# Kernel tuning notes

Hardware: AMD Instinct MI355X
Metric: run time of the kernel (lower is better)

## Reference

```python
import jax, jax.numpy as jnp
import numpy as np

FEATURE_DIM = 512
NUM_HEADS = 8
HEAD_DIM = FEATURE_DIM // NUM_HEADS
B, L = 4, 2048


def setup_inputs() -> dict:
    key = jax.random.key(0)
    ks = jax.random.split(key, 10)
    s = 1.0 / np.sqrt(FEATURE_DIM)
    inp = {
        "ppg": jax.random.normal(ks[0], (B, FEATURE_DIM, L), dtype=jnp.float32),
        "ecg": jax.random.normal(ks[1], (B, FEATURE_DIM, L), dtype=jnp.float32),
        "Wq": jax.random.uniform(ks[2], (FEATURE_DIM, FEATURE_DIM), jnp.float32, -s, s),
        "bq": jnp.zeros((FEATURE_DIM,), jnp.float32),
        "Wk": jax.random.uniform(ks[3], (FEATURE_DIM, FEATURE_DIM), jnp.float32, -s, s),
        "bk": jnp.zeros((FEATURE_DIM,), jnp.float32),
        "Wv": jax.random.uniform(ks[4], (FEATURE_DIM, FEATURE_DIM), jnp.float32, -s, s),
        "bv": jnp.zeros((FEATURE_DIM,), jnp.float32),
        "Wo": jax.random.uniform(ks[5], (FEATURE_DIM, FEATURE_DIM), jnp.float32, -s, s),
        "bo": jnp.zeros((FEATURE_DIM,), jnp.float32),
    }
    return inp


def reference(ppg, ecg, Wq, bq, Wk, bk, Wv, bv, Wo, bo):
    # ppg/ecg: (B, C, L) -> (B, L, C)
    x = jnp.transpose(ppg, (0, 2, 1))
    y = jnp.transpose(ecg, (0, 2, 1))
    q = x @ Wq.T + bq  # (B, L, C)
    k = y @ Wk.T + bk
    v = y @ Wv.T + bv
    # split heads: (B, H, L, D)
    def split(t):
        return jnp.transpose(t.reshape(B, L, NUM_HEADS, HEAD_DIM), (0, 2, 1, 3))
    qh, kh, vh = split(q), split(k), split(v)
    scores = jnp.einsum('bhqd,bhkd->bhqk', qh, kh) / jnp.sqrt(jnp.float32(HEAD_DIM))
    probs = jax.nn.softmax(scores, axis=-1)  # dropout is identity in eval mode
    ctx = jnp.einsum('bhqk,bhkd->bhqd', probs, vh)
    ctx = jnp.transpose(ctx, (0, 2, 1, 3)).reshape(B, L, FEATURE_DIM)
    out = ctx @ Wo.T + bo + x  # residual with transposed ppg
    return jnp.transpose(out, (0, 2, 1))  # (B, C, L)
```

## Files before the change

kernel.cpp:

```cpp
#include <hip/hip_runtime.h>
#include <hip/hip_bf16.h>

static constexpr int Bc = 4;
static constexpr int Lc = 2048;
static constexpr int Cc = 512;
static constexpr int Hc = 8;
static constexpr int Dc = 64;

using short8  = __attribute__((ext_vector_type(8))) short;
using float4v = __attribute__((ext_vector_type(4))) float;

static __device__ __forceinline__ unsigned short f2bf(float f) {
    __hip_bfloat16 h = __float2bfloat16(f);
    return *reinterpret_cast<unsigned short*>(&h);
}

__global__ __launch_bounds__(256) void prep_kernel(
    const float* __restrict__ ppg, const float* __restrict__ ecg,
    const float* __restrict__ Wq, const float* __restrict__ Wk,
    const float* __restrict__ Wv, const float* __restrict__ Wo,
    unsigned short* __restrict__ Xt_ppg, unsigned short* __restrict__ Xt_ecg,
    unsigned short* __restrict__ Wbf)
{
    __shared__ float Ts[64 * 69];
    const int task = blockIdx.x;
    const int tid  = threadIdx.x;

    if (task < 2048) {
        const int src = task >> 10;
        const int rem = task & 1023;
        const int b   = rem >> 8;
        const int c0  = ((rem >> 5) & 7) * 64;
        const int l0  = (rem & 31) * 64;
        const float* X = src ? ecg : ppg;
        unsigned short* Xt = src ? Xt_ecg : Xt_ppg;

        #pragma unroll
        for (int j = 0; j < 4; ++j) {
            int idx = tid + j * 256;
            int c = idx >> 4, l4 = idx & 15;
            float4 v = *(const float4*)(X + ((size_t)b * Cc + c0 + c) * Lc + l0 + l4 * 4);
            Ts[c * 69 + l4 * 4 + 0] = v.x;
            Ts[c * 69 + l4 * 4 + 1] = v.y;
            Ts[c * 69 + l4 * 4 + 2] = v.z;
            Ts[c * 69 + l4 * 4 + 3] = v.w;
        }
        __syncthreads();
        #pragma unroll
        for (int j = 0; j < 8; ++j) {
            int u = tid + j * 256;
            int l = u >> 5, p2 = u & 31;
            float a = Ts[(2 * p2) * 69 + l];
            float bb = Ts[(2 * p2 + 1) * 69 + l];
            ushort2 pk; pk.x = f2bf(a); pk.y = f2bf(bb);
            *(ushort2*)(Xt + ((size_t)b * Lc + l0 + l) * Cc + c0 + 2 * p2) = pk;
        }
    } else {
        const int wb   = task - 2048;
        const int widx = wb >> 7;
        const float* W = widx == 0 ? Wq : widx == 1 ? Wk : widx == 2 ? Wv : Wo;
        size_t off = (size_t)(wb & 127) * 2048 + (size_t)tid * 8;
        float4 v0 = *(const float4*)(W + off);
        float4 v1 = *(const float4*)(W + off + 4);
        unsigned short pk[8] = {f2bf(v0.x), f2bf(v0.y), f2bf(v0.z), f2bf(v0.w),
                                f2bf(v1.x), f2bf(v1.y), f2bf(v1.z), f2bf(v1.w)};
        *(short8*)(Wbf + (size_t)widx * Cc * Cc + off) = *(const short8*)pk;
    }
}

__global__ __launch_bounds__(256) void proj_kernel(
    const unsigned short* __restrict__ Xt_ppg,
    const unsigned short* __restrict__ Xt_ecg,
    const unsigned short* __restrict__ Wbf,
    const float* __restrict__ bq, const float* __restrict__ bk,
    const float* __restrict__ bv,
    unsigned short* __restrict__ Qw, unsigned short* __restrict__ Kw,
    unsigned short* __restrict__ Vtw)
{
    constexpr int LDW = 72;
    const int z = blockIdx.z, p = z >> 2, b = z & 3;
    const int l0 = blockIdx.x * 128, n0 = blockIdx.y * 128;
    const unsigned short* X = (p == 0) ? Xt_ppg : Xt_ecg;
    const unsigned short* W = Wbf + (size_t)p * Cc * Cc;
    const float* bias = (p == 0) ? bq : (p == 1) ? bk : bv;

    const int tid = threadIdx.x, wave = tid >> 6, lane = tid & 63;
    const int l16 = lane & 15, quad = lane >> 4;
    const int wr = wave >> 1, wc = wave & 1;

    __shared__ __align__(16) unsigned short At[128 * LDW];
    __shared__ __align__(16) unsigned short Bt[128 * LDW];

    float4v acc[4][4] = {};
    short8 areg[4], breg[4];

    const int srow = tid >> 3, sc8 = tid & 7;
    #pragma unroll
    for (int j = 0; j < 4; ++j) {
        areg[j] = *(const short8*)(X + ((size_t)b * Lc + l0 + srow + j * 32) * Cc + sc8 * 8);
        breg[j] = *(const short8*)(W + (size_t)(n0 + srow + j * 32) * Cc + sc8 * 8);
    }

    for (int c0 = 0; c0 < Cc; c0 += 64) {
        #pragma unroll
        for (int j = 0; j < 4; ++j) {
            *(short8*)&At[(srow + j * 32) * LDW + sc8 * 8] = areg[j];
            *(short8*)&Bt[(srow + j * 32) * LDW + sc8 * 8] = breg[j];
        }
        __syncthreads();

        if (c0 + 64 < Cc) {
            #pragma unroll
            for (int j = 0; j < 4; ++j) {
                areg[j] = *(const short8*)(X + ((size_t)b * Lc + l0 + srow + j * 32) * Cc
                                           + c0 + 64 + sc8 * 8);
                breg[j] = *(const short8*)(W + (size_t)(n0 + srow + j * 32) * Cc
                                           + c0 + 64 + sc8 * 8);
            }
        }

        const unsigned short* Am = (p < 2) ? At : Bt;
        const unsigned short* Bm = (p < 2) ? Bt : At;

        #pragma unroll
        for (int ks = 0; ks < 2; ++ks) {
            short8 bf[4];
            #pragma unroll
            for (int nt = 0; nt < 4; ++nt)
                bf[nt] = *(const short8*)&Bm[(wc * 64 + nt * 16 + l16) * LDW
                                             + ks * 32 + quad * 8];
            #pragma unroll
            for (int mt = 0; mt < 4; ++mt) {
                short8 af = *(const short8*)&Am[(wr * 64 + mt * 16 + l16) * LDW
                                                + ks * 32 + quad * 8];
                #pragma unroll
                for (int nt = 0; nt < 4; ++nt)
                    acc[mt][nt] = __builtin_amdgcn_mfma_f32_16x16x32_bf16(
                        af, bf[nt], acc[mt][nt], 0, 0, 0);
            }
        }
        __syncthreads();
    }

    if (p < 2) {
        const float sc = (p == 0) ? 0.18033688011112042f : 1.0f;
        unsigned short* dst = (p == 0) ? Qw : Kw;
        #pragma unroll
        for (int nt = 0; nt < 4; ++nt) {
            int n = n0 + wc * 64 + nt * 16 + l16;
            int h = n >> 6, d = n & 63;
            int bh = b * Hc + h;
            float bia = bias[n];
            #pragma unroll
            for (int mt = 0; mt < 4; ++mt) {
                #pragma unroll
                for (int r = 0; r < 4; ++r) {
                    int l = l0 + wr * 64 + mt * 16 + quad * 4 + r;
                    dst[((size_t)bh * Lc + l) * Dc + d] =
                        f2bf((acc[mt][nt][r] + bia) * sc);
                }
            }
        }
    } else {
        #pragma unroll
        for (int mt = 0; mt < 4; ++mt) {
            #pragma unroll
            for (int r = 0; r < 4; ++r) {
                int n = n0 + wr * 64 + mt * 16 + quad * 4 + r;
                int h = n >> 6, d = n & 63;
                int bh = b * Hc + h;
                float bia = bias[n];
                #pragma unroll
                for (int nt = 0; nt < 4; ++nt) {
                    int l = l0 + wc * 64 + nt * 16 + l16;
                    Vtw[((size_t)bh * Dc + d) * Lc + l] = f2bf(acc[mt][nt][r] + bia);
                }
            }
        }
    }
}

__global__ __launch_bounds__(256) void attn_mfma_kernel(
    const unsigned short* __restrict__ Qg,
    const unsigned short* __restrict__ Kg,
    const unsigned short* __restrict__ Vtg,
    unsigned short* __restrict__ ctx)
{
    constexpr int LDW = 72;
    const int bh   = blockIdx.y;
    const int q0   = blockIdx.x * 64;
    const int tid  = threadIdx.x;
    const int wave = tid >> 6;
    const int lane = tid & 63;
    const int l16  = lane & 15;
    const int quad = lane >> 4;

    __shared__ __align__(16) unsigned short Kt[64 * LDW];
    __shared__ __align__(16) unsigned short Vt[64 * LDW];
    __shared__ __align__(16) unsigned short PT[64 * LDW];

    const int srow = tid >> 3, sc8 = tid & 7;

    const unsigned short* Qb = Qg + ((size_t)bh * Lc + q0) * Dc;
    #pragma unroll
    for (int j = 0; j < 2; ++j)
        *(short8*)&PT[(srow + j * 32) * LDW + sc8 * 8] =
            *(const short8*)(Qb + (srow + j * 32) * Dc + sc8 * 8);
    __syncthreads();

    short8 qf[2];
    #pragma unroll
    for (int ks = 0; ks < 2; ++ks)
        qf[ks] = *(const short8*)&PT[(wave * 16 + l16) * LDW + ks * 32 + quad * 8];

    float4v O[4] = {};
    float lsum = 0.0f;

    const unsigned short* Kb0 = Kg + (size_t)bh * Lc * Dc;
    const unsigned short* Vb0 = Vtg + (size_t)bh * (Dc * Lc);

    short8 kreg[2], vreg[2];
    #pragma unroll
    for (int j = 0; j < 2; ++j) {
        kreg[j] = *(const short8*)(Kb0 + (size_t)(srow + j * 32) * Dc + sc8 * 8);
        vreg[j] = *(const short8*)(Vb0 + (size_t)(srow + j * 32) * Lc + sc8 * 8);
    }

    for (int kc = 0; kc < Lc; kc += 64) {
        #pragma unroll
        for (int j = 0; j < 2; ++j) {
            *(short8*)&Kt[(srow + j * 32) * LDW + sc8 * 8] = kreg[j];
            *(short8*)&Vt[(srow + j * 32) * LDW + sc8 * 8] = vreg[j];
        }
        __syncthreads();

        if (kc + 64 < Lc) {
            #pragma unroll
            for (int j = 0; j < 2; ++j) {
                kreg[j] = *(const short8*)(Kb0 + (size_t)(kc + 64 + srow + j * 32) * Dc
                                           + sc8 * 8);
                vreg[j] = *(const short8*)(Vb0 + (size_t)(srow + j * 32) * Lc
                                           + kc + 64 + sc8 * 8);
            }
        }

        float4v S[4];
        #pragma unroll
        for (int kt = 0; kt < 4; ++kt) S[kt] = (float4v){0.f, 0.f, 0.f, 0.f};
        #pragma unroll
        for (int ks = 0; ks < 2; ++ks) {
            #pragma unroll
            for (int kt = 0; kt < 4; ++kt) {
                short8 af = *(const short8*)&Kt[(kt * 16 + l16) * LDW
                                                + ks * 32 + quad * 8];
                S[kt] = __builtin_amdgcn_mfma_f32_16x16x32_bf16(
                    af, qf[ks], S[kt], 0, 0, 0);
            }
        }

        #pragma unroll
        for (int kt = 0; kt < 4; ++kt) {
            float p0 = __builtin_amdgcn_exp2f(S[kt][0]);
            float p1 = __builtin_amdgcn_exp2f(S[kt][1]);
            float p2 = __builtin_amdgcn_exp2f(S[kt][2]);
            float p3 = __builtin_amdgcn_exp2f(S[kt][3]);
            lsum += (p0 + p1) + (p2 + p3);
            ushort4 pk;
            pk.x = f2bf(p0); pk.y = f2bf(p1); pk.z = f2bf(p2); pk.w = f2bf(p3);
            *(ushort4*)&PT[(wave * 16 + l16) * LDW + kt * 16 + quad * 4] = pk;
        }

        #pragma unroll
        for (int ks = 0; ks < 2; ++ks) {
            short8 pf = *(const short8*)&PT[(wave * 16 + l16) * LDW
                                            + ks * 32 + quad * 8];
            #pragma unroll
            for (int dt = 0; dt < 4; ++dt) {
                short8 vf = *(const short8*)&Vt[(dt * 16 + l16) * LDW
                                                + ks * 32 + quad * 8];
                O[dt] = __builtin_amdgcn_mfma_f32_16x16x32_bf16(
                    vf, pf, O[dt], 0, 0, 0);
            }
        }
        __syncthreads();
    }

    float t = lsum;
    t += __shfl_xor(t, 16, 64);
    t += __shfl_xor(t, 32, 64);
    const float inv_l = 1.0f / t;

    const int b = bh >> 3, h = bh & 7;
    const int q = q0 + wave * 16 + l16;
    #pragma unroll
    for (int dt = 0; dt < 4; ++dt) {
        ushort4 pk;
        pk.x = f2bf(O[dt][0] * inv_l);
        pk.y = f2bf(O[dt][1] * inv_l);
        pk.z = f2bf(O[dt][2] * inv_l);
        pk.w = f2bf(O[dt][3] * inv_l);
        *(ushort4*)(ctx + ((size_t)b * Lc + q) * Cc
                    + h * Dc + dt * 16 + quad * 4) = pk;
    }
}

__global__ __launch_bounds__(256) void outproj_kernel(
    const unsigned short* __restrict__ ctx, const unsigned short* __restrict__ Wo_bf,
    const float* __restrict__ bo, const float* __restrict__ ppg,
    float* __restrict__ out)
{
    constexpr int LDW = 72;
    const int b = blockIdx.z;
    const int l0 = blockIdx.x * 128, n0 = blockIdx.y * 64;
    const int tid = threadIdx.x, wave = tid >> 6, lane = tid & 63;
    const int l16 = lane & 15, quad = lane >> 4;

    __shared__ __align__(16) unsigned short At[64 * LDW];
    __shared__ __align__(16) unsigned short Bt[128 * LDW];

    float4v acc[4][2] = {};
    short8 areg[2], breg[4];

    const int srow = tid >> 3, sc8 = tid & 7;
    #pragma unroll
    for (int j = 0; j < 2; ++j)
        areg[j] = *(const short8*)(Wo_bf + (size_t)(n0 + srow + j * 32) * Cc + sc8 * 8);
    #pragma unroll
    for (int j = 0; j < 4; ++j)
        breg[j] = *(const short8*)(ctx + ((size_t)b * Lc + l0 + srow + j * 32) * Cc + sc8 * 8);

    for (int c0 = 0; c0 < Cc; c0 += 64) {
        #pragma unroll
        for (int j = 0; j < 2; ++j)
            *(short8*)&At[(srow + j * 32) * LDW + sc8 * 8] = areg[j];
        #pragma unroll
        for (int j = 0; j < 4; ++j)
            *(short8*)&Bt[(srow + j * 32) * LDW + sc8 * 8] = breg[j];
        __syncthreads();

        if (c0 + 64 < Cc) {
            #pragma unroll
            for (int j = 0; j < 2; ++j)
                areg[j] = *(const short8*)(Wo_bf + (size_t)(n0 + srow + j * 32) * Cc
                                           + c0 + 64 + sc8 * 8);
            #pragma unroll
            for (int j = 0; j < 4; ++j)
                breg[j] = *(const short8*)(ctx + ((size_t)b * Lc + l0 + srow + j * 32) * Cc
                                           + c0 + 64 + sc8 * 8);
        }

        #pragma unroll
        for (int ks = 0; ks < 2; ++ks) {
            short8 bf[2];
            #pragma unroll
            for (int nt = 0; nt < 2; ++nt)
                bf[nt] = *(const short8*)&Bt[(wave * 32 + nt * 16 + l16) * LDW
                                             + ks * 32 + quad * 8];
            #pragma unroll
            for (int mt = 0; mt < 4; ++mt) {
                short8 af = *(const short8*)&At[(mt * 16 + l16) * LDW
                                                + ks * 32 + quad * 8];
                #pragma unroll
                for (int nt = 0; nt < 2; ++nt)
                    acc[mt][nt] = __builtin_amdgcn_mfma_f32_16x16x32_bf16(
                        af, bf[nt], acc[mt][nt], 0, 0, 0);
            }
        }
        __syncthreads();
    }

    #pragma unroll
    for (int mt = 0; mt < 4; ++mt) {
        #pragma unroll
        for (int r = 0; r < 4; ++r) {
            int n = n0 + mt * 16 + quad * 4 + r;
            float bia = bo[n];
            #pragma unroll
            for (int nt = 0; nt < 2; ++nt) {
                int l = l0 + wave * 32 + nt * 16 + l16;
                size_t oidx = ((size_t)b * Cc + n) * Lc + l;
                out[oidx] = acc[mt][nt][r] + bia + ppg[oidx];
            }
        }
    }
}

extern "C" void kernel_launch(void* const* d_in, const int* in_sizes, int n_in,
                              void* d_out, int out_size, void* d_ws, size_t ws_size,
                              hipStream_t stream) {
    const float* ppg = (const float*)d_in[0];
    const float* ecg = (const float*)d_in[1];
    const float* Wq  = (const float*)d_in[2];
    const float* bq  = (const float*)d_in[3];
    const float* Wk  = (const float*)d_in[4];
    const float* bk  = (const float*)d_in[5];
    const float* Wv  = (const float*)d_in[6];
    const float* bv  = (const float*)d_in[7];
    const float* Wo  = (const float*)d_in[8];
    const float* bo  = (const float*)d_in[9];
    float* out = (float*)d_out;

    const size_t plane = (size_t)Bc * Lc * Cc;
    unsigned short* Xt_ppg = (unsigned short*)d_ws;
    unsigned short* Xt_ecg = Xt_ppg + plane;
    unsigned short* Wbf    = Xt_ecg + plane;
    unsigned short* Qw     = Wbf + (size_t)4 * Cc * Cc;
    unsigned short* Kw     = Qw + plane;
    unsigned short* Vtw    = Kw + plane;
    unsigned short* ctx    = Vtw + plane;

    prep_kernel<<<2560, 256, 0, stream>>>(ppg, ecg, Wq, Wk, Wv, Wo,
                                          Xt_ppg, Xt_ecg, Wbf);

    dim3 g1(Lc / 128, Cc / 128, 3 * Bc);
    proj_kernel<<<g1, 256, 0, stream>>>(Xt_ppg, Xt_ecg, Wbf, bq, bk, bv,
                                        Qw, Kw, Vtw);

    dim3 g2(Lc / 64, Bc * Hc);
    attn_mfma_kernel<<<g2, 256, 0, stream>>>(Qw, Kw, Vtw, ctx);

    dim3 g3(Lc / 128, Cc / 64, Bc);
    outproj_kernel<<<g3, 256, 0, stream>>>(ctx, Wbf + (size_t)3 * Cc * Cc,
                                           bo, ppg, out);
}
```

Before: 193.9 us.

## Split attention keys across two blocks and double query rows per wave

The attention kernel now handles 128 query rows per block, with two 16-row query tiles per wave, so each K and V fragment loaded from LDS feeds two MFMAs. The key range is also split in half across a new grid dimension. Each half writes unnormalized fp32 partial outputs and row sums to workspace, and a new combine kernel adds the halves, normalizes and writes bf16 ctx. The aim is more MFMA work per LDS read while keeping the block count unchanged. The cost is extra fp32 global traffic, an additional kernel launch, higher register pressure and a larger workspace footprint that aliases earlier buffers.

New measurement: 184.7 us. -4.8%, faster.

```diff
diff --git a/kernel.cpp b/kernel.cpp
--- a/kernel.cpp
+++ b/kernel.cpp
@@ -180,53 +180,59 @@
     }
 }
 
-__global__ __launch_bounds__(256) void attn_mfma_kernel(
+__global__ __launch_bounds__(256, 4) void attn_mfma_kernel(
     const unsigned short* __restrict__ Qg,
     const unsigned short* __restrict__ Kg,
     const unsigned short* __restrict__ Vtg,
-    unsigned short* __restrict__ ctx)
+    float* __restrict__ O0, float* __restrict__ O1,
+    float* __restrict__ lpart)
 {
     constexpr int LDW = 72;
-    const int bh   = blockIdx.y;
-    const int q0   = blockIdx.x * 64;
-    const int tid  = threadIdx.x;
-    const int wave = tid >> 6;
-    const int lane = tid & 63;
-    const int l16  = lane & 15;
-    const int quad = lane >> 4;
+    const int bh    = blockIdx.y;
+    const int split = blockIdx.z;
+    const int q0    = blockIdx.x * 128;
+    const int tid   = threadIdx.x;
+    const int wave  = tid >> 6;
+    const int lane  = tid & 63;
+    const int l16   = lane & 15;
+    const int quad  = lane >> 4;
 
     __shared__ __align__(16) unsigned short Kt[64 * LDW];
     __shared__ __align__(16) unsigned short Vt[64 * LDW];
-    __shared__ __align__(16) unsigned short PT[64 * LDW];
+    __shared__ __align__(16) unsigned short PT[128 * LDW];
 
     const int srow = tid >> 3, sc8 = tid & 7;
 
     const unsigned short* Qb = Qg + ((size_t)bh * Lc + q0) * Dc;
     #pragma unroll
-    for (int j = 0; j < 2; ++j)
+    for (int j = 0; j < 4; ++j)
         *(short8*)&PT[(srow + j * 32) * LDW + sc8 * 8] =
             *(const short8*)(Qb + (srow + j * 32) * Dc + sc8 * 8);
     __syncthreads();
 
-    short8 qf[2];
-    #pragma unroll
-    for (int ks = 0; ks < 2; ++ks)
-        qf[ks] = *(const short8*)&PT[(wave * 16 + l16) * LDW + ks * 32 + quad * 8];
-
-    float4v O[4] = {};
-    float lsum = 0.0f;
+    short8 qf[2][2];
+    #pragma unroll
+    for (int qt = 0; qt < 2; ++qt)
+        #pragma unroll
+        for (int ks = 0; ks < 2; ++ks)
+            qf[qt][ks] = *(const short8*)&PT[(wave * 32 + qt * 16 + l16) * LDW
+                                             + ks * 32 + quad * 8];
+
+    float4v O[2][4] = {};
+    float lsum[2] = {0.0f, 0.0f};
 
     const unsigned short* Kb0 = Kg + (size_t)bh * Lc * Dc;
     const unsigned short* Vb0 = Vtg + (size_t)bh * (Dc * Lc);
+    const int kbase = split * (Lc / 2);
 
     short8 kreg[2], vreg[2];
     #pragma unroll
     for (int j = 0; j < 2; ++j) {
-        kreg[j] = *(const short8*)(Kb0 + (size_t)(srow + j * 32) * Dc + sc8 * 8);
-        vreg[j] = *(const short8*)(Vb0 + (size_t)(srow + j * 32) * Lc + sc8 * 8);
-    }
-
-    for (int kc = 0; kc < Lc; kc += 64) {
+        kreg[j] = *(const short8*)(Kb0 + (size_t)(kbase + srow + j * 32) * Dc + sc8 * 8);
+        vreg[j] = *(const short8*)(Vb0 + (size_t)(srow + j * 32) * Lc + kbase + sc8 * 8);
+    }
+
+    for (int kc = kbase; kc < kbase + Lc / 2; kc += 64) {
         #pragma unroll
         for (int j = 0; j < 2; ++j) {
             *(short8*)&Kt[(srow + j * 32) * LDW + sc8 * 8] = kreg[j];
@@ -234,7 +240,7 @@
         }
         __syncthreads();
 
-        if (kc + 64 < Lc) {
+        if (kc + 64 < kbase + Lc / 2) {
             #pragma unroll
             for (int j = 0; j < 2; ++j) {
                 kreg[j] = *(const short8*)(Kb0 + (size_t)(kc + 64 + srow + j * 32) * Dc
@@ -244,64 +250,107 @@
             }
         }
 
-        float4v S[4];
-        #pragma unroll
-        for (int kt = 0; kt < 4; ++kt) S[kt] = (float4v){0.f, 0.f, 0.f, 0.f};
+        float4v S[4][2];
+        #pragma unroll
+        for (int kt = 0; kt < 4; ++kt)
+            #pragma unroll
+            for (int qt = 0; qt < 2; ++qt)
+                S[kt][qt] = (float4v){0.f, 0.f, 0.f, 0.f};
         #pragma unroll
         for (int ks = 0; ks < 2; ++ks) {
             #pragma unroll
             for (int kt = 0; kt < 4; ++kt) {
                 short8 af = *(const short8*)&Kt[(kt * 16 + l16) * LDW
                                                 + ks * 32 + quad * 8];
-                S[kt] = __builtin_amdgcn_mfma_f32_16x16x32_bf16(
-                    af, qf[ks], S[kt], 0, 0, 0);
-            }
-        }
-
-        #pragma unroll
-        for (int kt = 0; kt < 4; ++kt) {
-            float p0 = __builtin_amdgcn_exp2f(S[kt][0]);
-            float p1 = __builtin_amdgcn_exp2f(S[kt][1]);
-            float p2 = __builtin_amdgcn_exp2f(S[kt][2]);
-            float p3 = __builtin_amdgcn_exp2f(S[kt][3]);
-            lsum += (p0 + p1) + (p2 + p3);
-            ushort4 pk;
-            pk.x = f2bf(p0); pk.y = f2bf(p1); pk.z = f2bf(p2); pk.w = f2bf(p3);
-            *(ushort4*)&PT[(wave * 16 + l16) * LDW + kt * 16 + quad * 4] = pk;
+                #pragma unroll
+                for (int qt = 0; qt < 2; ++qt)
+                    S[kt][qt] = __builtin_amdgcn_mfma_f32_16x16x32_bf16(
+                        af, qf[qt][ks], S[kt][qt], 0, 0, 0);
+            }
+        }
+
+        #pragma unroll
+        for (int qt = 0; qt < 2; ++qt) {
+            #pragma unroll
+            for (int kt = 0; kt < 4; ++kt) {
+                float p0 = __builtin_amdgcn_exp2f(S[kt][qt][0]);
+                float p1 = __builtin_amdgcn_exp2f(S[kt][qt][1]);
+                float p2 = __builtin_amdgcn_exp2f(S[kt][qt][2]);
+                float p3 = __builtin_amdgcn_exp2f(S[kt][qt][3]);
+                lsum[qt] += (p0 + p1) + (p2 + p3);
+                ushort4 pk;
+                pk.x = f2bf(p0); pk.y = f2bf(p1); pk.z = f2bf(p2); pk.w = f2bf(p3);
+                *(ushort4*)&PT[(wave * 32 + qt * 16 + l16) * LDW
+                               + kt * 16 + quad * 4] = pk;
+            }
         }
 
         #pragma unroll
         for (int ks = 0; ks < 2; ++ks) {
-            short8 pf = *(const short8*)&PT[(wave * 16 + l16) * LDW
-                                            + ks * 32 + quad * 8];
+            short8 pf[2];
+            #pragma unroll
+            for (int qt = 0; qt < 2; ++qt)
+                pf[qt] = *(const short8*)&PT[(wave * 32 + qt * 16 + l16) * LDW
+                                             + ks * 32 + quad * 8];
             #pragma unroll
             for (int dt = 0; dt < 4; ++dt) {
                 short8 vf = *(const short8*)&Vt[(dt * 16 + l16) * LDW
                                                 + ks * 32 + quad * 8];
-                O[dt] = __builtin_amdgcn_mfma_f32_16x16x32_bf16(
-                    vf, pf, O[dt], 0, 0, 0);
-            }
-        }
-        __syncthreads();
-    }
-
-    float t = lsum;
-    t += __shfl_xor(t, 16, 64);
-    t += __shfl_xor(t, 32, 64);
-    const float inv_l = 1.0f / t;
+                #pragma unroll
+                for (int qt = 0; qt < 2; ++qt)
+                    O[qt][dt] = __builtin_amdgcn_mfma_f32_16x16x32_bf16(
+                        pf[qt], vf, O[qt][dt], 0, 0, 0);
+            }
+        }
+        __syncthreads();
+    }
 
     const int b = bh >> 3, h = bh & 7;
-    const int q = q0 + wave * 16 + l16;
-    #pragma unroll
-    for (int dt = 0; dt < 4; ++dt) {
-        ushort4 pk;
-        pk.x = f2bf(O[dt][0] * inv_l);
-        pk.y = f2bf(O[dt][1] * inv_l);
-        pk.z = f2bf(O[dt][2] * inv_l);
-        pk.w = f2bf(O[dt][3] * inv_l);
-        *(ushort4*)(ctx + ((size_t)b * Lc + q) * Cc
-                    + h * Dc + dt * 16 + quad * 4) = pk;
-    }
+    float* Op = split ? O1 : O0;
+    float* lp = lpart + (size_t)split * (Bc * Hc) * Lc + (size_t)bh * Lc;
+
+    #pragma unroll
+    for (int qt = 0; qt < 2; ++qt) {
+        float t = lsum[qt];
+        t += __shfl_xor(t, 16, 64);
+        t += __shfl_xor(t, 32, 64);
+        if (quad == 0)
+            lp[q0 + wave * 32 + qt * 16 + l16] = t;
+        #pragma unroll
+        for (int dt = 0; dt < 4; ++dt) {
+            #pragma unroll
+            for (int r = 0; r < 4; ++r) {
+                int q = q0 + wave * 32 + qt * 16 + quad * 4 + r;
+                Op[((size_t)b * Lc + q) * Cc + h * Dc + dt * 16 + l16] =
+                    O[qt][dt][r];
+            }
+        }
+    }
+}
+
+__global__ __launch_bounds__(256) void combine_kernel(
+    const float* __restrict__ O0, const float* __restrict__ O1,
+    const float* __restrict__ lpart, unsigned short* __restrict__ ctx)
+{
+    const int row = blockIdx.x;
+    const int b   = row >> 11;
+    const int l   = row & (Lc - 1);
+    const int tid = threadIdx.x;
+    const int c   = tid * 2;
+    const int h   = c >> 6;
+
+    const size_t lplane = (size_t)(Bc * Hc) * Lc;
+    float denom = lpart[(size_t)(b * Hc + h) * Lc + l]
+                + lpart[lplane + (size_t)(b * Hc + h) * Lc + l];
+    float inv = 1.0f / denom;
+
+    size_t off = (size_t)row * Cc + c;
+    float2 a = *(const float2*)(O0 + off);
+    float2 bb = *(const float2*)(O1 + off);
+    ushort2 pk;
+    pk.x = f2bf((a.x + bb.x) * inv);
+    pk.y = f2bf((a.y + bb.y) * inv);
+    *(ushort2*)(ctx + off) = pk;
 }
 
 __global__ __launch_bounds__(256) void outproj_kernel(
@@ -400,14 +449,18 @@
     const float* bo  = (const float*)d_in[9];
     float* out = (float*)d_out;
 
-    const size_t plane = (size_t)Bc * Lc * Cc;
-    unsigned short* Xt_ppg = (unsigned short*)d_ws;
-    unsigned short* Xt_ecg = Xt_ppg + plane;
-    unsigned short* Wbf    = Xt_ecg + plane;
-    unsigned short* Qw     = Wbf + (size_t)4 * Cc * Cc;
-    unsigned short* Kw     = Qw + plane;
-    unsigned short* Vtw    = Kw + plane;
-    unsigned short* ctx    = Vtw + plane;
+    unsigned short* base   = (unsigned short*)d_ws;
+    const size_t M = 1024 * 1024;
+    unsigned short* Xt_ppg = base;
+    unsigned short* Xt_ecg = base + 4 * M;
+    unsigned short* Wbf    = base + 8 * M;
+    unsigned short* Qw     = base + 9 * M;
+    unsigned short* Kw     = base + 13 * M;
+    unsigned short* Vtw    = base + 17 * M;
+    float* Opart0 = (float*)base;
+    float* Opart1 = (float*)(base + 21 * M);
+    float* lpart  = (float*)(base + 29 * M);
+    unsigned short* ctx = Qw;
 
     prep_kernel<<<2560, 256, 0, stream>>>(ppg, ecg, Wq, Wk, Wv, Wo,
                                           Xt_ppg, Xt_ecg, Wbf);
@@ -416,8 +469,10 @@
     proj_kernel<<<g1, 256, 0, stream>>>(Xt_ppg, Xt_ecg, Wbf, bq, bk, bv,
                                         Qw, Kw, Vtw);
 
-    dim3 g2(Lc / 64, Bc * Hc);
-    attn_mfma_kernel<<<g2, 256, 0, stream>>>(Qw, Kw, Vtw, ctx);
+    dim3 g2(Lc / 128, Bc * Hc, 2);
+    attn_mfma_kernel<<<g2, 256, 0, stream>>>(Qw, Kw, Vtw, Opart0, Opart1, lpart);
+
+    combine_kernel<<<Bc * Lc, 256, 0, stream>>>(Opart0, Opart1, lpart, ctx);
 
     dim3 g3(Lc / 128, Cc / 64, Bc);
     outproj_kernel<<<g3, 256, 0, stream>>>(ctx, Wbf + (size_t)3 * Cc * Cc,
```
